# Performance work log

Measured on AMD Instinct MI355X. Metric: run time of the kernel, lower is better.

## Reference

```python
import jax, jax.numpy as jnp
import numpy as np

B, L, D, H, DK, DV = 2, 2048, 1024, 16, 64, 64


def setup_inputs() -> dict:
    key = jax.random.key(0)
    ks = jax.random.split(key, 9)
    s = 0.02
    q = jax.random.normal(ks[0], (B, L, D), dtype=jnp.float32)
    k = jax.random.normal(ks[1], (B, L, D), dtype=jnp.float32)
    v = jax.random.normal(ks[2], (B, L, D), dtype=jnp.float32)
    # causal mask: mask==0 positions are masked out (matches masked_fill(mask==0, -1e9))
    mask = jnp.broadcast_to(jnp.tril(jnp.ones((L, L), dtype=jnp.int32)), (B, L, L))
    Wq = jax.random.normal(ks[3], (D, H * DK), dtype=jnp.float32) * s
    Wk = jax.random.normal(ks[4], (D, H * DK), dtype=jnp.float32) * s
    Wv = jax.random.normal(ks[5], (D, H * DV), dtype=jnp.float32) * s
    Wfc = jax.random.normal(ks[6], (H * DV, D), dtype=jnp.float32) * s
    gamma = jnp.ones((D,), dtype=jnp.float32)
    beta = jnp.zeros((D,), dtype=jnp.float32)
    return {"q": q, "k": k, "v": v, "Wq": Wq, "Wk": Wk, "Wv": Wv,
            "Wfc": Wfc, "gamma": gamma, "beta": beta, "mask": mask}


def reference(q, k, v, Wq, Wk, Wv, Wfc, gamma, beta, mask):
    residual = q
    # project and split heads: [B, H, L, dk]
    qh = (q @ Wq).reshape(B, L, H, DK).transpose(0, 2, 1, 3)
    kh = (k @ Wk).reshape(B, L, H, DK).transpose(0, 2, 1, 3)
    vh = (v @ Wv).reshape(B, L, H, DV).transpose(0, 2, 1, 3)
    temperature = jnp.asarray(DK, jnp.float32) ** 0.5
    scores = jnp.einsum('bhqd,bhkd->bhqk', qh / temperature, kh)  # [B,H,L,L]
    scores = jnp.where(mask[:, None, :, :] == 0, jnp.float32(-1e9), scores)
    attn = jax.nn.softmax(scores, axis=-1)  # dropout = identity (eval)
    out = jnp.einsum('bhqk,bhkd->bhqd', attn, vh)
    out = out.transpose(0, 2, 1, 3).reshape(B, L, H * DV)
    out = out @ Wfc + residual  # dropout = identity (eval)
    # LayerNorm, eps=1e-6
    mu = jnp.mean(out, axis=-1, keepdims=True)
    var = jnp.mean((out - mu) ** 2, axis=-1, keepdims=True)
    out = (out - mu) * jax.lax.rsqrt(var + 1e-6) * gamma + beta
    return out, attn
```

## Files before the change

### kernel.cpp

```cpp
#include <hip/hip_runtime.h>
#include <hip/hip_bf16.h>

#define NB 2
#define NL 2048
#define ND 1024
#define NH 16
#define NDK 64

typedef float fx4 __attribute__((ext_vector_type(4)));
typedef short sx8 __attribute__((ext_vector_type(8)));
typedef short sx4 __attribute__((ext_vector_type(4)));

static __device__ __forceinline__ short f2bf(float x) {
  __hip_bfloat16 h = __float2bfloat16(x);
  short s;
  __builtin_memcpy(&s, &h, 2);
  return s;
}

static __device__ __forceinline__ float ex2(float x) {
  float r; asm("v_exp_f32 %0, %1" : "=v"(r) : "v"(x)); return r;
}

static __device__ __forceinline__ void lds_barrier() {
  __asm__ volatile("s_waitcnt lgkmcnt(0)" ::: "memory");
  __builtin_amdgcn_s_barrier();
}

__global__ __launch_bounds__(256) void wt_kernel(
    const float* __restrict__ Wq, const float* __restrict__ Wk,
    const float* __restrict__ Wv, const float* __restrict__ Wfc,
    short* __restrict__ wt)
{
  const float* W = (blockIdx.z==0)?Wq:(blockIdx.z==1)?Wk:(blockIdx.z==2)?Wv:Wfc;
  float sc = (blockIdx.z==0) ? 0.18033688011112042f : 1.0f;
  short* out = wt + (size_t)blockIdx.z*1024*1024;
  int n0 = blockIdx.x*64, k0 = blockIdx.y*64;
  __shared__ float t[64][65];
  int tid = threadIdx.x;
  int kr = tid>>2, ns = (tid&3)*16;
  #pragma unroll
  for (int i=0;i<4;i++){
    fx4 v = *(const fx4*)(W + (size_t)(k0+kr)*1024 + n0 + ns + i*4);
    t[kr][ns+i*4+0]=v[0]; t[kr][ns+i*4+1]=v[1];
    t[kr][ns+i*4+2]=v[2]; t[kr][ns+i*4+3]=v[3];
  }
  __syncthreads();
  int nr = tid>>2, ks = (tid&3)*16;
  sx8 o0,o1;
  #pragma unroll
  for (int i=0;i<8;i++){ o0[i]=f2bf(t[ks+i][nr]*sc); o1[i]=f2bf(t[ks+8+i][nr]*sc); }
  *(sx8*)(out + (size_t)(n0+nr)*1024 + k0 + ks)     = o0;
  *(sx8*)(out + (size_t)(n0+nr)*1024 + k0 + ks + 8) = o1;
}

__global__ __launch_bounds__(256) void cast_kernel(
    const float* __restrict__ q, const float* __restrict__ k,
    const float* __restrict__ v, short* __restrict__ qb,
    short* __restrict__ kb, short* __restrict__ vb)
{
  const float* src = (blockIdx.y==0)?q:(blockIdx.y==1)?k:v;
  short* dst = (blockIdx.y==0)?qb:(blockIdx.y==1)?kb:vb;
  size_t base = ((size_t)blockIdx.x*256 + threadIdx.x)*8;
  fx4 a = *(const fx4*)(src+base), b = *(const fx4*)(src+base+4);
  sx8 o;
  o[0]=f2bf(a[0]); o[1]=f2bf(a[1]); o[2]=f2bf(a[2]); o[3]=f2bf(a[3]);
  o[4]=f2bf(b[0]); o[5]=f2bf(b[1]); o[6]=f2bf(b[2]); o[7]=f2bf(b[3]);
  *(sx8*)(dst+base) = o;
}

__global__ __launch_bounds__(256) void gemm_kernel(
    const short* __restrict__ qb, const short* __restrict__ kb,
    const short* __restrict__ vb, const short* __restrict__ ao,
    const float* __restrict__ q, const short* __restrict__ wt,
    short* __restrict__ qh, short* __restrict__ kh, short* __restrict__ vtb,
    float* __restrict__ preln, int mode_base)
{
  int mode = mode_base + blockIdx.z;
  const short* Ab = (mode==0)?qb:(mode==1)?kb:(mode==2)?vb:ao;
  const short* Bw = wt + (size_t)mode*1048576;
  int m0 = blockIdx.y*128, n0 = blockIdx.x*128;
  __shared__ short Al[128*64];
  __shared__ short Bl[128*64];
  int tid = threadIdx.x;
  int w = tid>>6, l = tid&63, lr = l>>4, lc = l&15;
  int wm = w>>1, wn = w&1;
  int grow = l>>3, gcol = (l&7)*8;

  fx4 acc[4][4];
  #pragma unroll
  for (int i=0;i<4;i++)
    #pragma unroll
    for (int j=0;j<4;j++) acc[i][j] = (fx4)0.0f;

  for (int kb2=0; kb2<1024; kb2+=64) {
    #pragma unroll
    for (int p=0;p<4;p++){
      int rb = w*32 + p*8;
      __builtin_amdgcn_global_load_lds(
        (const __attribute__((address_space(1))) int*)(Ab + (size_t)(m0+rb+grow)*1024 + kb2 + gcol),
        (__attribute__((address_space(3))) int*)&Al[rb*64], 16, 0, 0);
      __builtin_amdgcn_global_load_lds(
        (const __attribute__((address_space(1))) int*)(Bw + (size_t)(n0+rb+grow)*1024 + kb2 + gcol),
        (__attribute__((address_space(3))) int*)&Bl[rb*64], 16, 0, 0);
    }
    __syncthreads();
    #pragma unroll
    for (int kk=0;kk<2;kk++){
      sx8 af[4], bfr[4];
      int oct = kk*4 + lr;
      #pragma unroll
      for (int i=0;i<4;i++){
        af[i]  = *(const sx8*)&Al[(wm*64 + i*16 + lc)*64 + oct*8];
        bfr[i] = *(const sx8*)&Bl[(wn*64 + i*16 + lc)*64 + oct*8];
      }
      #pragma unroll
      for (int i=0;i<4;i++)
        #pragma unroll
        for (int j=0;j<4;j++)
          acc[i][j] = __builtin_amdgcn_mfma_f32_16x16x32_bf16(af[i], bfr[j], acc[i][j], 0,0,0);
    }
    __syncthreads();
  }

  #pragma unroll
  for (int i=0;i<4;i++){
    int mrow0 = m0 + wm*64 + i*16 + lr*4;
    #pragma unroll
    for (int j=0;j<4;j++){
      int n = n0 + wn*64 + j*16 + lc;
      if (mode<=1) {
        short* dst = (mode==0)?qh:kh;
        int hh = n>>6, d = n&63;
        #pragma unroll
        for (int r=0;r<4;r++){
          int mr = mrow0 + r; int bb = mr>>11, lp = mr&2047;
          dst[((size_t)(bb*16+hh)*2048 + lp)*64 + d] = f2bf(acc[i][j][r]);
        }
      } else if (mode==2) {
        int hh = n>>6, d = n&63;
        int bb = mrow0>>11, lp = mrow0&2047;
        sx4 pv;
        #pragma unroll
        for (int r=0;r<4;r++) pv[r] = f2bf(acc[i][j][r]);
        *(sx4*)&vtb[((size_t)(bb*16+hh)*64 + d)*2048 + lp] = pv;
      } else {
        #pragma unroll
        for (int r=0;r<4;r++){
          int mr = mrow0 + r;
          preln[(size_t)mr*1024 + n] = acc[i][j][r] + q[(size_t)mr*1024 + n];
        }
      }
    }
  }
}

__global__ __launch_bounds__(256) void attn_kernel(
    const short* __restrict__ qh, const short* __restrict__ kh,
    const short* __restrict__ vt, short* __restrict__ ao,
    float* __restrict__ attn)
{
  int qt = 31 - (int)blockIdx.x;
  int bh = blockIdx.y;
  int qbase = qt*64;
  int tid = threadIdx.x, w = tid>>6, l = tid&63, lr = l>>4, lc = l&15;
  int qrow0 = qbase + w*16;
  int qrow_l = qrow0 + lc;
  int kend = qrow0 + 16;
  int knlim = (w + 2) & ~1;

  float* arow = attn + (size_t)bh*NL*NL;
  const short* qhb = qh + (size_t)bh*NL*64;
  const short* khb = kh + (size_t)bh*NL*64;
  const short* vtb = vt + (size_t)bh*64*NL;

  sx8 Qf0 = *(const sx8*)&qhb[(size_t)qrow_l*64 + lr*8];
  sx8 Qf1 = *(const sx8*)&qhb[(size_t)qrow_l*64 + 32 + lr*8];

  __shared__ short Kl[2][64][64];
  __shared__ short Vl[2][64][64];
  __shared__ short pl[4][16][40];

  int idx0 = w*64 + l;
  int idx1 = 256 + w*64 + l;
  int rA = idx0>>3, oA = idx0&7, rB = idx1>>3, oB = idx1&7;
  int ntile = qt + 1;

  {
    sx8 ka = *(const sx8*)&khb[(size_t)rA*64 + oA*8];
    sx8 kb = *(const sx8*)&khb[(size_t)rB*64 + oB*8];
    *(sx8*)&Kl[0][rA][(oA^(rA&7))*8] = ka;
    *(sx8*)&Kl[0][rB][(oB^(rB&7))*8] = kb;
  }
  lds_barrier();

  float ls = 0.0f;
  int buf = 0;
  #pragma unroll 1
  for (int t=0; t<ntile; t++){
    bool have_next = (t+1) < ntile;
    sx8 ka, kb;
    if (have_next){
      int nb = (t+1)*64;
      ka = *(const sx8*)&khb[(size_t)(nb+rA)*64 + oA*8];
      kb = *(const sx8*)&khb[(size_t)(nb+rB)*64 + oB*8];
    }
    bool diag = (t == qt);
    #pragma unroll
    for (int kn=0; kn<4; kn++){
      if (diag && kn > w) continue;
      int rk = kn*16 + lc;
      sx8 k0 = *(const sx8*)&Kl[buf][rk][((lr  ^(rk&7))*8)];
      sx8 k1 = *(const sx8*)&Kl[buf][rk][(((lr+4)^(rk&7))*8)];
      fx4 s = (fx4)0.0f;
      s = __builtin_amdgcn_mfma_f32_16x16x32_bf16(k0, Qf0, s, 0,0,0);
      s = __builtin_amdgcn_mfma_f32_16x16x32_bf16(k1, Qf1, s, 0,0,0);
      if (!diag || kn < w) {
        ls += (ex2(s[0]) + ex2(s[1])) + (ex2(s[2]) + ex2(s[3]));
      } else {
        int key0 = t*64 + kn*16 + lr*4;
        #pragma unroll
        for (int r=0;r<4;r++)
          ls += (key0 + r <= qrow_l) ? ex2(s[r]) : 0.0f;
      }
    }
    if (have_next){
      int nbuf = buf ^ 1;
      *(sx8*)&Kl[nbuf][rA][(oA^(rA&7))*8] = ka;
      *(sx8*)&Kl[nbuf][rB][(oB^(rB&7))*8] = kb;
    }
    lds_barrier();
    buf ^= 1;
  }
  ls += __shfl_xor(ls, 16, 64);
  ls += __shfl_xor(ls, 32, 64);
  float inv = 1.0f / ls;

  {
    int fs = ((kend + 31) >> 5) << 5;
    fx4 z = (fx4)0.0f;
    #pragma unroll 1
    for (int r=0; r<16; r++){
      float* rp = &arow[(size_t)(qrow0+r)*NL];
      for (int c = fs + l*4; c < NL; c += 256)
        __builtin_nontemporal_store(z, (fx4*)&rp[c]);
    }
  }

  {
    sx8 ka = *(const sx8*)&khb[(size_t)rA*64 + oA*8];
    sx8 kb = *(const sx8*)&khb[(size_t)rB*64 + oB*8];
    sx8 va = *(const sx8*)&vtb[(size_t)rA*NL + oA*8];
    sx8 vb = *(const sx8*)&vtb[(size_t)rB*NL + oB*8];
    *(sx8*)&Kl[0][rA][(oA^(rA&7))*8] = ka;
    *(sx8*)&Kl[0][rB][(oB^(rB&7))*8] = kb;
    *(sx8*)&Vl[0][rA][(oA^(rA&7))*8] = va;
    *(sx8*)&Vl[0][rB][(oB^(rB&7))*8] = vb;
  }
  lds_barrier();

  fx4 O[4];
  #pragma unroll
  for (int n=0;n<4;n++) O[n] = (fx4)0.0f;

  buf = 0;
  #pragma unroll 1
  for (int t=0; t<ntile; t++){
    int tb = t*64;
    bool have_next = (t+1) < ntile;
    sx8 ka, kb, va, vb;
    if (have_next){
      int nb = tb + 64;
      ka = *(const sx8*)&khb[(size_t)(nb+rA)*64 + oA*8];
      kb = *(const sx8*)&khb[(size_t)(nb+rB)*64 + oB*8];
      va = *(const sx8*)&vtb[(size_t)rA*NL + nb + oA*8];
      vb = *(const sx8*)&vtb[(size_t)rB*NL + nb + oB*8];
    }
    bool diag = (t == qt);
    #pragma unroll
    for (int kn=0; kn<4; kn++){
      fx4 p;
      if (!diag || kn <= w) {
        int rk = kn*16 + lc;
        sx8 k0 = *(const sx8*)&Kl[buf][rk][((lr  ^(rk&7))*8)];
        sx8 k1 = *(const sx8*)&Kl[buf][rk][(((lr+4)^(rk&7))*8)];
        fx4 s = (fx4)0.0f;
        s = __builtin_amdgcn_mfma_f32_16x16x32_bf16(k0, Qf0, s, 0,0,0);
        s = __builtin_amdgcn_mfma_f32_16x16x32_bf16(k1, Qf1, s, 0,0,0);
        if (!diag || kn < w) {
          #pragma unroll
          for (int r=0;r<4;r++) p[r] = ex2(s[r]) * inv;
        } else {
          int key0 = tb + kn*16 + lr*4;
          #pragma unroll
          for (int r=0;r<4;r++)
            p[r] = (key0 + r <= qrow_l) ? ex2(s[r]) * inv : 0.0f;
        }
      } else {
        p = (fx4)0.0f;
      }
      if (!diag || kn < knlim)
        __builtin_nontemporal_store(p, (fx4*)&arow[(size_t)qrow_l*NL + tb + kn*16 + lr*4]);
      sx4 pbv;
      #pragma unroll
      for (int r=0;r<4;r++) pbv[r] = f2bf(p[r]);
      *(sx4*)&pl[w][lc][(kn&1)*16 + lr*4] = pbv;
      if (kn & 1){
        sx8 pf = *(const sx8*)&pl[w][lc][lr*8];
        int t2 = kn>>1;
        #pragma unroll
        for (int n=0;n<4;n++){
          int rv = n*16 + lc;
          sx8 vf = *(const sx8*)&Vl[buf][rv][(((t2*4+lr)^(rv&7))*8)];
          O[n] = __builtin_amdgcn_mfma_f32_16x16x32_bf16(pf, vf, O[n], 0,0,0);
        }
      }
    }
    if (have_next){
      int nbuf = buf ^ 1;
      *(sx8*)&Kl[nbuf][rA][(oA^(rA&7))*8] = ka;
      *(sx8*)&Kl[nbuf][rB][(oB^(rB&7))*8] = kb;
      *(sx8*)&Vl[nbuf][rA][(oA^(rA&7))*8] = va;
      *(sx8*)&Vl[nbuf][rB][(oB^(rB&7))*8] = vb;
    }
    lds_barrier();
    buf ^= 1;
  }

  int bb = bh>>4, hh = bh&15;
  #pragma unroll
  for (int n=0;n<4;n++)
    #pragma unroll
    for (int r=0;r<4;r++)
      ao[((size_t)bb*NL + qrow0 + lr*4 + r)*1024 + hh*64 + n*16 + lc] = f2bf(O[n][r]);
}

__global__ __launch_bounds__(256) void ln_kernel(
    const float* __restrict__ preln, const float* __restrict__ gamma,
    const float* __restrict__ beta, float* __restrict__ out)
{
  int row = blockIdx.x, tid = threadIdx.x;
  fx4 x = *(const fx4*)&preln[(size_t)row*1024 + tid*4];
  float s  = x[0]+x[1]+x[2]+x[3];
  float sq = x[0]*x[0]+x[1]*x[1]+x[2]*x[2]+x[3]*x[3];
  #pragma unroll
  for (int off=1; off<64; off<<=1){
    s  += __shfl_xor(s,  off, 64);
    sq += __shfl_xor(sq, off, 64);
  }
  __shared__ float rs[4], rq[4];
  int w = tid>>6, l = tid&63;
  if (l==0){ rs[w]=s; rq[w]=sq; }
  __syncthreads();
  s  = rs[0]+rs[1]+rs[2]+rs[3];
  sq = rq[0]+rq[1]+rq[2]+rq[3];
  float mean = s*(1.0f/1024.0f);
  float var  = sq*(1.0f/1024.0f) - mean*mean;
  float rstd = rsqrtf(var + 1e-6f);
  fx4 g = *(const fx4*)&gamma[tid*4];
  fx4 b = *(const fx4*)&beta[tid*4];
  fx4 y;
  #pragma unroll
  for (int i=0;i<4;i++) y[i] = (x[i]-mean)*rstd*g[i] + b[i];
  *(fx4*)&out[(size_t)row*1024 + tid*4] = y;
}

extern "C" void kernel_launch(void* const* d_in, const int* in_sizes, int n_in,
                              void* d_out, int out_size, void* d_ws, size_t ws_size,
                              hipStream_t stream) {
  const float* q    = (const float*)d_in[0];
  const float* k    = (const float*)d_in[1];
  const float* v    = (const float*)d_in[2];
  const float* Wq   = (const float*)d_in[3];
  const float* Wk   = (const float*)d_in[4];
  const float* Wv   = (const float*)d_in[5];
  const float* Wfc  = (const float*)d_in[6];
  const float* gamma= (const float*)d_in[7];
  const float* beta = (const float*)d_in[8];

  float* out  = (float*)d_out;
  float* attn = out + (size_t)NB*NL*ND;

  char* ws = (char*)d_ws;
  short* wt    = (short*)(ws);
  short* qb    = (short*)(ws + ((size_t) 8<<20));
  short* kb    = (short*)(ws + ((size_t)16<<20));
  short* vb    = (short*)(ws + ((size_t)24<<20));
  short* qh    = (short*)(ws + ((size_t)32<<20));
  short* kh    = (short*)(ws + ((size_t)40<<20));
  short* vtb   = (short*)(ws + ((size_t)48<<20));
  short* ao    = (short*)(ws + ((size_t)56<<20));
  float* preln = (float*)(ws + ((size_t) 8<<20));

  wt_kernel<<<dim3(16,16,4), 256, 0, stream>>>(Wq, Wk, Wv, Wfc, wt);
  cast_kernel<<<dim3(2048,3), 256, 0, stream>>>(q, k, v, qb, kb, vb);
  gemm_kernel<<<dim3(8,32,3), 256, 0, stream>>>(qb,kb,vb,ao, q, wt, qh,kh,vtb, preln, 0);
  attn_kernel<<<dim3(32,32), 256, 0, stream>>>(qh, kh, vtb, ao, attn);
  gemm_kernel<<<dim3(8,32,1), 256, 0, stream>>>(qb,kb,vb,ao, q, wt, qh,kh,vtb, preln, 3);
  ln_kernel<<<4096, 256, 0, stream>>>(preln, gamma, beta, out);
}
```

Before: 284.5 us.

## Stage attention probabilities in LDS for row-coalesced stores; read V from global

Probabilities are staged per warp in a 256-column LDS buffer as bf16 and written out as full contiguous row segments every four key tiles. The masked-zero tail fill is realigned to these 256-column chunks. V tiles are loaded straight from global memory into registers instead of being double-buffered through LDS. The intent is better-coalesced writes of the large attn output and less LDS traffic, at the cost of rounding the stored attn matrix to bf16 precision and extra register pressure.

```diff
diff --git a/kernel.cpp b/kernel.cpp
--- a/kernel.cpp
+++ b/kernel.cpp
@@ -16,6 +16,13 @@
   short s;
   __builtin_memcpy(&s, &h, 2);
   return s;
+}
+
+static __device__ __forceinline__ float bf2f(short s) {
+  unsigned u = ((unsigned)(unsigned short)s) << 16;
+  float f;
+  __builtin_memcpy(&f, &u, 4);
+  return f;
 }
 
 static __device__ __forceinline__ float ex2(float x) {
@@ -167,7 +174,6 @@
   int qrow0 = qbase + w*16;
   int qrow_l = qrow0 + lc;
   int kend = qrow0 + 16;
-  int knlim = (w + 2) & ~1;
 
   float* arow = attn + (size_t)bh*NL*NL;
   const short* qhb = qh + (size_t)bh*NL*64;
@@ -178,8 +184,7 @@
   sx8 Qf1 = *(const sx8*)&qhb[(size_t)qrow_l*64 + 32 + lr*8];
 
   __shared__ short Kl[2][64][64];
-  __shared__ short Vl[2][64][64];
-  __shared__ short pl[4][16][40];
+  __shared__ short pstage[4][16][264];
 
   int idx0 = w*64 + l;
   int idx1 = 256 + w*64 + l;
@@ -237,25 +242,18 @@
   float inv = 1.0f / ls;
 
   {
-    int fs = ((kend + 31) >> 5) << 5;
+    int fs = ((ntile*64 + 255) >> 8) << 8;
     fx4 z = (fx4)0.0f;
-    #pragma unroll 1
-    for (int r=0; r<16; r++){
-      float* rp = &arow[(size_t)(qrow0+r)*NL];
+    for (int r = w; r < 64; r += 4)
       for (int c = fs + l*4; c < NL; c += 256)
-        __builtin_nontemporal_store(z, (fx4*)&rp[c]);
-    }
+        __builtin_nontemporal_store(z, (fx4*)&arow[(size_t)(qbase+r)*NL + c]);
   }
 
   {
     sx8 ka = *(const sx8*)&khb[(size_t)rA*64 + oA*8];
     sx8 kb = *(const sx8*)&khb[(size_t)rB*64 + oB*8];
-    sx8 va = *(const sx8*)&vtb[(size_t)rA*NL + oA*8];
-    sx8 vb = *(const sx8*)&vtb[(size_t)rB*NL + oB*8];
     *(sx8*)&Kl[0][rA][(oA^(rA&7))*8] = ka;
     *(sx8*)&Kl[0][rB][(oB^(rB&7))*8] = kb;
-    *(sx8*)&Vl[0][rA][(oA^(rA&7))*8] = va;
-    *(sx8*)&Vl[0][rB][(oB^(rB&7))*8] = vb;
   }
   lds_barrier();
 
@@ -268,15 +266,22 @@
   for (int t=0; t<ntile; t++){
     int tb = t*64;
     bool have_next = (t+1) < ntile;
-    sx8 ka, kb, va, vb;
+    sx8 ka, kb;
     if (have_next){
       int nb = tb + 64;
       ka = *(const sx8*)&khb[(size_t)(nb+rA)*64 + oA*8];
       kb = *(const sx8*)&khb[(size_t)(nb+rB)*64 + oB*8];
-      va = *(const sx8*)&vtb[(size_t)rA*NL + nb + oA*8];
-      vb = *(const sx8*)&vtb[(size_t)rB*NL + nb + oB*8];
-    }
+    }
+    sx8 Vv[8];
+    #pragma unroll
+    for (int t2=0;t2<2;t2++)
+      #pragma unroll
+      for (int n=0;n<4;n++)
+        Vv[t2*4+n] = *(const sx8*)&vtb[(size_t)(n*16+lc)*NL + tb + t2*32 + lr*8];
+
     bool diag = (t == qt);
+    int sb = tb & ~255;
+    int scol = tb - sb;
     #pragma unroll
     for (int kn=0; kn<4; kn++){
       fx4 p;
@@ -299,29 +304,36 @@
       } else {
         p = (fx4)0.0f;
       }
-      if (!diag || kn < knlim)
-        __builtin_nontemporal_store(p, (fx4*)&arow[(size_t)qrow_l*NL + tb + kn*16 + lr*4]);
       sx4 pbv;
       #pragma unroll
       for (int r=0;r<4;r++) pbv[r] = f2bf(p[r]);
-      *(sx4*)&pl[w][lc][(kn&1)*16 + lr*4] = pbv;
+      *(sx4*)&pstage[w][lc][scol + kn*16 + lr*4] = pbv;
       if (kn & 1){
-        sx8 pf = *(const sx8*)&pl[w][lc][lr*8];
-        int t2 = kn>>1;
-        #pragma unroll
-        for (int n=0;n<4;n++){
-          int rv = n*16 + lc;
-          sx8 vf = *(const sx8*)&Vl[buf][rv][(((t2*4+lr)^(rv&7))*8)];
-          O[n] = __builtin_amdgcn_mfma_f32_16x16x32_bf16(pf, vf, O[n], 0,0,0);
-        }
+        sx8 pf = *(const sx8*)&pstage[w][lc][scol + (kn>>1)*32 + lr*8];
+        #pragma unroll
+        for (int n=0;n<4;n++)
+          O[n] = __builtin_amdgcn_mfma_f32_16x16x32_bf16(pf, Vv[(kn>>1)*4+n], O[n], 0,0,0);
       }
     }
     if (have_next){
       int nbuf = buf ^ 1;
       *(sx8*)&Kl[nbuf][rA][(oA^(rA&7))*8] = ka;
       *(sx8*)&Kl[nbuf][rB][(oB^(rB&7))*8] = kb;
-      *(sx8*)&Vl[nbuf][rA][(oA^(rA&7))*8] = va;
-      *(sx8*)&Vl[nbuf][rB][(oB^(rB&7))*8] = vb;
+    }
+    if ((((tb + 64) & 255) == 0) || !have_next){
+      if (!have_next){
+        int zc0 = tb + 64 - sb;
+        for (int cc = zc0; cc < 256; cc += 16)
+          *(sx4*)&pstage[w][l>>2][cc + (l&3)*4] = (sx4)(short)0;
+      }
+      #pragma unroll 1
+      for (int r=0; r<16; r++){
+        sx4 pb4 = *(const sx4*)&pstage[w][r][l*4];
+        fx4 o;
+        #pragma unroll
+        for (int i=0;i<4;i++) o[i] = bf2f(pb4[i]);
+        __builtin_nontemporal_store(o, (fx4*)&arow[(size_t)(qrow0+r)*NL + sb + l*4]);
+      }
     }
     lds_barrier();
     buf ^= 1;
```

New measurement: 320.2 us. 1.13x slower.
